# Kernel tuning notes

Measured on AMD Instinct MI355X. Metric: run time of the kernel, lower is better.

Reference implementation:

```python
import jax, jax.numpy as jnp
import numpy as np
from jax import lax

EPS = 1e-7   # keras.backend.epsilon()
NEG = -1e30  # log-space -inf surrogate


def setup_inputs() -> dict:
    key = jax.random.key(0)
    k1, k2 = jax.random.split(key)
    B, T, C, L = 512, 1024, 256, 64
    logits = jax.random.uniform(k1, (B, T, C), dtype=jnp.float32)
    y_pred = logits / jnp.sum(logits, axis=-1, keepdims=True)  # valid probability rows
    y_true = jax.random.randint(k2, (B, L), 0, C - 1, dtype=jnp.int32)  # avoid blank=C-1
    return {"y_true": y_true, "y_pred": y_pred}


def _ctc_loss(y_pred, y_true):
    # y_pred: [B,T,C] probabilities; y_true: [B,L] labels; blank = C-1,
    # input_length = T and label_length = L for all batch elements (as in the module).
    B, T, C = y_pred.shape
    L = y_true.shape[1]
    S = 2 * L + 1
    blank = C - 1
    lp = jnp.log(y_pred + EPS)  # [B,T,C]

    # extended label sequence: blank, l1, blank, l2, ..., blank  -> [B,S]
    ext = jnp.full((B, S), blank, dtype=jnp.int32).at[:, 1::2].set(y_true.astype(jnp.int32))
    # per-step emission log-probs gathered on the extended sequence: [T,B,S]
    lp_ext = jnp.take_along_axis(lp, ext[:, None, :], axis=2).transpose(1, 0, 2)

    # skip transition (s-2 -> s) allowed iff ext[s] != blank and ext[s] != ext[s-2]
    ext_sm2 = jnp.pad(ext, ((0, 0), (2, 0)), constant_values=blank)[:, :S]
    allow_skip = (ext != blank) & (ext != ext_sm2)  # [B,S]

    alpha0 = jnp.full((B, S), NEG, dtype=lp.dtype)
    alpha0 = alpha0.at[:, 0].set(lp_ext[0, :, 0]).at[:, 1].set(lp_ext[0, :, 1])

    def step(alpha, lp_t):
        a1 = alpha
        a2 = jnp.pad(alpha, ((0, 0), (1, 0)), constant_values=NEG)[:, :S]
        a3 = jnp.where(allow_skip,
                       jnp.pad(alpha, ((0, 0), (2, 0)), constant_values=NEG)[:, :S],
                       NEG)
        m = jnp.maximum(jnp.maximum(a1, a2), a3)
        new = m + jnp.log(jnp.exp(a1 - m) + jnp.exp(a2 - m) + jnp.exp(a3 - m)) + lp_t
        return new, None

    alpha, _ = lax.scan(step, alpha0, lp_ext[1:])
    # sequence ends on final blank or final label
    total = jnp.logaddexp(alpha[:, S - 1], alpha[:, S - 2])
    return -total[:, None]  # [B,1], matching expand_dims in ctc_batch_cost


def reference(y_true, y_pred):
    return _ctc_loss(y_pred, y_true)
```

## Files before the change

### kernel.cpp

```cpp
#include <hip/hip_runtime.h>


#define EPS 1e-7f
#define NEG -1e30f

constexpr int Bb = 512;
constexpr int Tt = 1024;
constexpr int Cc = 256;
constexpr int Ll = 64;
constexpr int BLANK = Cc - 1;
constexpr int DPF = 16;

__global__ __launch_bounds__(64) void ctc_fwd_kernel(
    const int* __restrict__ y_true,
    const float* __restrict__ y_pred,
    float* __restrict__ out)
{
    const int b = blockIdx.x;
    const int lane = threadIdx.x;

    const float* __restrict__ row0 = y_pred + (size_t)b * Tt * Cc;

    const int lab = y_true[b * Ll + lane];
    const int lab_prev = __shfl_up(lab, 1);
    const bool allow = (lane == 0) ? true : (lab != lab_prev);

    {
    }
    const float pb0 = row0[BLANK];
    const float pl0 = row0[lab];
    float ae = (lane == 0) ? __logf(pb0 + EPS) : NEG;
    float ao = (lane == 0) ? __logf(pl0 + EPS) : NEG;
    float a128 = NEG;

    float pl[DPF], pb[DPF];
#pragma unroll
    for (int j = 0; j < DPF; ++j) {
        const int t = 1 + j;
        pl[j] = row0[t * Cc + lab];
        pb[j] = row0[t * Cc + BLANK];
    }

    int t = 1;

    auto step = [&](int slot, bool do_prefetch) {
        const float lpl = __logf(pl[slot] + EPS);
        const float lpb = __logf(pb[slot] + EPS);
        if (do_prefetch) {
            const int tn = t + DPF;
            if (tn < Tt) {
                pl[slot] = row0[tn * Cc + lab];
                pb[slot] = row0[tn * Cc + BLANK];
            }
        }
        float ao_up = __shfl_up(ao, 1);
        if (lane == 0) ao_up = NEG;

        const float m2 = fmaxf(ae, ao_up);
        const float ne =
            m2 + __logf(__expf(ae - m2) + __expf(ao_up - m2)) + lpb;

        const float a3 = allow ? ao_up : NEG;
        const float m3 = fmaxf(fmaxf(ao, ae), a3);
        const float no =
            m3 +
            __logf(__expf(ao - m3) + __expf(ae - m3) + __expf(a3 - m3)) +
            lpl;

        const float m1 = fmaxf(a128, ao);
        const float n128 =
            m1 + __logf(__expf(a128 - m1) + __expf(ao - m1)) + lpb;

        ae = ne;
        ao = no;
        a128 = n128;
        ++t;
    };

    for (int chunk = 0; chunk < (Tt - 1) / DPF; ++chunk) {
#pragma unroll
        for (int k = 0; k < DPF; ++k) {
            step(k, true);
        }
    }
#pragma unroll
    for (int k = 0; k < (Tt - 1) % DPF; ++k) {
        step(k, false);
    }

    if (lane == 63) {
        const float m = fmaxf(a128, ao);
        const float total = m + __logf(__expf(a128 - m) + __expf(ao - m));
        out[b] = -total;
    }
}

extern "C" void kernel_launch(void* const* d_in, const int* in_sizes, int n_in,
                              void* d_out, int out_size, void* d_ws,
                              size_t ws_size, hipStream_t stream) {
    const int* y_true = (const int*)d_in[0];
    const float* y_pred = (const float*)d_in[1];
    float* out = (float*)d_out;

    ctc_fwd_kernel<<<dim3(Bb), dim3(64), 0, stream>>>(y_true, y_pred, out);
}
```

Baseline: 804.8 us.

## Stream whole rows into an LDS ring via global_load_lds DMA

Swaps the per-lane register prefetch of two gathered scalars per timestep for a 32-slot LDS ring. Each step DMA-loads a full contiguous 1 KB probability row with global_load_lds, and s_waitcnt vmcnt(31) keeps 31 rows in flight. The goal is coalesced, deeper-pipelined loads that hide global latency on the serial recurrence. In exchange it moves the whole row instead of two scattered elements, relies on manual vmcnt accounting, and has no barrier between the DMA writes and the LDS reads, which is single-wave only.

```diff
diff --git a/kernel.cpp b/kernel.cpp
--- a/kernel.cpp
+++ b/kernel.cpp
@@ -1,4 +1,5 @@
 #include <hip/hip_runtime.h>
+#include <stdint.h>
 
 
 #define EPS 1e-7f
@@ -9,7 +10,16 @@
 constexpr int Cc = 256;
 constexpr int Ll = 64;
 constexpr int BLANK = Cc - 1;
-constexpr int DPF = 16;
+constexpr int D = 32;
+
+#define WAITVM31() asm volatile("s_waitcnt vmcnt(31)" ::: "memory")
+
+__device__ __forceinline__ void dma_row(const float* __restrict__ g,
+                                        float* l) {
+    __builtin_amdgcn_global_load_lds(
+        (const __attribute__((address_space(1))) void*)g,
+        (__attribute__((address_space(3))) void*)l, 16, 0, 0);
+}
 
 __global__ __launch_bounds__(64) void ctc_fwd_kernel(
     const int* __restrict__ y_true,
@@ -21,38 +31,34 @@
 
     const float* __restrict__ row0 = y_pred + (size_t)b * Tt * Cc;
 
+    __shared__ float ring[D * Cc];
+
     const int lab = y_true[b * Ll + lane];
     const int lab_prev = __shfl_up(lab, 1);
     const bool allow = (lane == 0) ? true : (lab != lab_prev);
 
-    {
-    }
-    const float pb0 = row0[BLANK];
-    const float pl0 = row0[lab];
+    for (int t0 = 0; t0 < D; ++t0)
+        dma_row(row0 + t0 * Cc + lane * 4, &ring[t0 * Cc]);
+
+    WAITVM31();
+    const float pl0 = ring[lab];
+    const float pb0 = ring[BLANK];
     float ae = (lane == 0) ? __logf(pb0 + EPS) : NEG;
     float ao = (lane == 0) ? __logf(pl0 + EPS) : NEG;
     float a128 = NEG;
 
-    float pl[DPF], pb[DPF];
-#pragma unroll
-    for (int j = 0; j < DPF; ++j) {
-        const int t = 1 + j;
-        pl[j] = row0[t * Cc + lab];
-        pb[j] = row0[t * Cc + BLANK];
-    }
+    dma_row(row0 + D * Cc + lane * 4, &ring[0]);
+    WAITVM31();
+    float glA = ring[1 * Cc + lab];
+    float gbA = ring[1 * Cc + BLANK];
+    dma_row(row0 + (D + 1) * Cc + lane * 4, &ring[1 * Cc]);
+    WAITVM31();
+    float glB = ring[2 * Cc + lab];
+    float gbB = ring[2 * Cc + BLANK];
 
-    int t = 1;
-
-    auto step = [&](int slot, bool do_prefetch) {
-        const float lpl = __logf(pl[slot] + EPS);
-        const float lpb = __logf(pb[slot] + EPS);
-        if (do_prefetch) {
-            const int tn = t + DPF;
-            if (tn < Tt) {
-                pl[slot] = row0[tn * Cc + lab];
-                pb[slot] = row0[tn * Cc + BLANK];
-            }
-        }
+    auto update = [&](float gl, float gb) {
+        const float lpl = __logf(gl + EPS);
+        const float lpb = __logf(gb + EPS);
         float ao_up = __shfl_up(ao, 1);
         if (lane == 0) ao_up = NEG;
 
@@ -74,24 +80,35 @@
         ae = ne;
         ao = no;
         a128 = n128;
-        ++t;
     };
 
-    for (int chunk = 0; chunk < (Tt - 1) / DPF; ++chunk) {
-#pragma unroll
-        for (int k = 0; k < DPF; ++k) {
-            step(k, true);
+    for (int t = 1; t <= Tt - 3; t += 2) {
+        update(glA, gbA);
+        {
+            const int tn = min(t + 1 + D, Tt - 1);
+            dma_row(row0 + tn * Cc + lane * 4,
+                    &ring[((t + 1) & (D - 1)) * Cc]);
+            WAITVM31();
+            const int s = (t + 2) & (D - 1);
+            glA = ring[s * Cc + lab];
+            gbA = ring[s * Cc + BLANK];
+        }
+        update(glB, gbB);
+        {
+            const int tn = min(t + 2 + D, Tt - 1);
+            dma_row(row0 + tn * Cc + lane * 4,
+                    &ring[((t + 2) & (D - 1)) * Cc]);
+            WAITVM31();
+            const int s = (t + 3) & (D - 1);
+            glB = ring[s * Cc + lab];
+            gbB = ring[s * Cc + BLANK];
         }
     }
-#pragma unroll
-    for (int k = 0; k < (Tt - 1) % DPF; ++k) {
-        step(k, false);
-    }
+    update(glA, gbA);
 
     if (lane == 63) {
         const float m = fmaxf(a128, ao);
-        const float total = m + __logf(__expf(a128 - m) + __expf(ao - m));
-        out[b] = -total;
+        out[b] = -(m + __logf(__expf(a128 - m) + __expf(ao - m)));
     }
 }
 
```

Result: no change. 800.1 us (-0.6%).

## Split CTC into parallel log-gather pass and compact sequential scan

Applied to the files above, without the earlier changes.

Adds a massively parallel pre-pass that streams y_pred with coalesced float4 loads into shared memory, computes log-probabilities for the label and blank columns, and writes them to a compact workspace. The scan kernel then reads these contiguous values instead of doing scattered gathers across 1KB rows, and no longer computes logs inside the serial recurrence. The cost is an extra kernel launch and a 128MB workspace round-trip, in exchange for full-bandwidth reads of the input and a shorter latency-bound scan loop.

```diff
diff --git a/kernel.cpp b/kernel.cpp
--- a/kernel.cpp
+++ b/kernel.cpp
@@ -1,4 +1,5 @@
 #include <hip/hip_runtime.h>
+#include <stdint.h>
 
 
 #define EPS 1e-7f
@@ -11,46 +12,76 @@
 constexpr int BLANK = Cc - 1;
 constexpr int DPF = 16;
 
-__global__ __launch_bounds__(64) void ctc_fwd_kernel(
+__global__ __launch_bounds__(256) void ctc_gather_kernel(
     const int* __restrict__ y_true,
     const float* __restrict__ y_pred,
+    float* __restrict__ G,
+    float* __restrict__ Bk)
+{
+    const int blk = blockIdx.x;
+    const int b = blk >> 8;
+    const int tg = blk & 255;
+    const int t0 = tg * 4;
+    const int tid = threadIdx.x;
+    const int w = tid >> 6;
+    const int lane = tid & 63;
+
+    __shared__ float rows[4 * Cc];
+
+    const float4* __restrict__ src =
+        (const float4*)(y_pred + ((size_t)b * Tt + t0) * Cc);
+    ((float4*)rows)[tid] = src[tid];
+
+    const int lab = y_true[b * Ll + lane];
+    __syncthreads();
+
+    const int t = t0 + w;
+    const float v = __logf(rows[w * Cc + lab] + EPS);
+    G[((size_t)b * Tt + t) * 64 + lane] = v;
+    if (lane == 0)
+        Bk[b * Tt + t] = __logf(rows[w * Cc + BLANK] + EPS);
+}
+
+__global__ __launch_bounds__(64) void ctc_scan_kernel(
+    const int* __restrict__ y_true,
+    const float* __restrict__ G,
+    const float* __restrict__ Bk,
     float* __restrict__ out)
 {
     const int b = blockIdx.x;
     const int lane = threadIdx.x;
 
-    const float* __restrict__ row0 = y_pred + (size_t)b * Tt * Cc;
+    const float* __restrict__ g = G + (size_t)b * Tt * 64;
+    const float* __restrict__ bk = Bk + (size_t)b * Tt;
 
     const int lab = y_true[b * Ll + lane];
     const int lab_prev = __shfl_up(lab, 1);
     const bool allow = (lane == 0) ? true : (lab != lab_prev);
 
-    {
-    }
-    const float pb0 = row0[BLANK];
-    const float pl0 = row0[lab];
-    float ae = (lane == 0) ? __logf(pb0 + EPS) : NEG;
-    float ao = (lane == 0) ? __logf(pl0 + EPS) : NEG;
+    const float g0 = g[lane];
+    const float b0 = bk[0];
+    float ae = (lane == 0) ? b0 : NEG;
+    float ao = (lane == 0) ? g0 : NEG;
     float a128 = NEG;
 
     float pl[DPF], pb[DPF];
 #pragma unroll
     for (int j = 0; j < DPF; ++j) {
         const int t = 1 + j;
-        pl[j] = row0[t * Cc + lab];
-        pb[j] = row0[t * Cc + BLANK];
+        pl[j] = g[(size_t)t * 64 + lane];
+        pb[j] = bk[t];
     }
 
     int t = 1;
 
     auto step = [&](int slot, bool do_prefetch) {
-        const float lpl = __logf(pl[slot] + EPS);
-        const float lpb = __logf(pb[slot] + EPS);
+        const float lpl = pl[slot];
+        const float lpb = pb[slot];
         if (do_prefetch) {
             const int tn = t + DPF;
             if (tn < Tt) {
-                pl[slot] = row0[tn * Cc + lab];
-                pb[slot] = row0[tn * Cc + BLANK];
+                pl[slot] = g[(size_t)tn * 64 + lane];
+                pb[slot] = bk[tn];
             }
         }
         float ao_up = __shfl_up(ao, 1);
@@ -79,19 +110,14 @@
 
     for (int chunk = 0; chunk < (Tt - 1) / DPF; ++chunk) {
 #pragma unroll
-        for (int k = 0; k < DPF; ++k) {
-            step(k, true);
-        }
+        for (int k = 0; k < DPF; ++k) step(k, true);
     }
 #pragma unroll
-    for (int k = 0; k < (Tt - 1) % DPF; ++k) {
-        step(k, false);
-    }
+    for (int k = 0; k < (Tt - 1) % DPF; ++k) step(k, false);
 
     if (lane == 63) {
         const float m = fmaxf(a128, ao);
-        const float total = m + __logf(__expf(a128 - m) + __expf(ao - m));
-        out[b] = -total;
+        out[b] = -(m + __logf(__expf(a128 - m) + __expf(ao - m)));
     }
 }
 
@@ -102,5 +128,10 @@
     const float* y_pred = (const float*)d_in[1];
     float* out = (float*)d_out;
 
-    ctc_fwd_kernel<<<dim3(Bb), dim3(64), 0, stream>>>(y_true, y_pred, out);
+    float* G = (float*)d_ws;
+    float* Bk = (float*)((char*)d_ws + (size_t)Bb * Tt * 64 * sizeof(float));
+
+    ctc_gather_kernel<<<dim3(Bb * (Tt / 4)), dim3(256), 0, stream>>>(
+        y_true, y_pred, G, Bk);
+    ctc_scan_kernel<<<dim3(Bb), dim3(64), 0, stream>>>(y_true, G, Bk, out);
 }
```

After: 874.4 us. +8.7%, slower.
